# Optimization experiments

Measured on AMD Instinct MI355X. Metric: run time of the kernel, lower is better.

The kernel has to match this reference:

```python
import jax, jax.numpy as jnp
from jax import lax
import numpy as np

B, S, V, E, H, K = 128, 512, 32000, 128, 128, 32  # H = hidden_dim//2 per direction
START, END = 30, 31


def _lstm_dir(x, h0, c0, W_ih, W_hh, b):
    # x: [S, B, E]; PyTorch gate order: i, f, g, o
    def step(carry, xt):
        h, c = carry
        gates = xt @ W_ih.T + h @ W_hh.T + b  # [B, 4H]
        i, f, g, o = jnp.split(gates, 4, axis=1)
        c = jax.nn.sigmoid(f) * c + jax.nn.sigmoid(i) * jnp.tanh(g)
        h = jax.nn.sigmoid(o) * jnp.tanh(c)
        return (h, c), h
    _, hs = lax.scan(step, (h0, c0), x)
    return hs  # [S, B, H]


def _get_features(sentence, embed_table, W_ih_f, W_hh_f, b_ih_f, b_hh_f,
                  W_ih_b, W_hh_b, b_ih_b, b_hh_b, W_out, b_out, h0, c0):
    emb = embed_table[sentence]            # [B, S, E]
    x = emb.transpose(1, 0, 2)             # [S, B, E]
    hf = _lstm_dir(x, h0[0], c0[0], W_ih_f, W_hh_f, b_ih_f + b_hh_f)
    hb = _lstm_dir(x[::-1], h0[1], c0[1], W_ih_b, W_hh_b, b_ih_b + b_hh_b)[::-1]
    out = jnp.concatenate([hf, hb], axis=-1).transpose(1, 0, 2)  # [B, S, 2H]
    return out @ W_out.T + b_out           # [B, S, K]


def _numerator(feats, tags, transitions):
    b = tags.shape[0]
    start = jnp.full((b, 1), START, dtype=tags.dtype)
    ext = jnp.concatenate([start, tags], axis=1)  # [B, S+1]
    trans = transitions[ext[:, :-1], ext[:, 1:]].sum(axis=1)
    emit = jnp.take_along_axis(feats, tags[:, :, None], axis=2)[..., 0].sum(axis=1)
    return trans + emit + transitions[tags[:, -1], END]


def _denominator(feats, transitions):
    b, _, k = feats.shape
    init = jnp.full((b, k), -10000.0, feats.dtype).at[:, START].set(0.0)
    def step(alpha, feat):
        # alpha[b, prev]; transitions[next, prev] (as in the torch code)
        new = jax.nn.logsumexp(alpha[:, None, :] + transitions[None, :, :], axis=2) + feat
        return new, None
    alpha, _ = lax.scan(step, init, feats.transpose(1, 0, 2))
    return jax.nn.logsumexp(alpha + transitions[:, END][None, :], axis=1)


def setup_inputs():
    key = jax.random.key(0)
    ks = jax.random.split(key, 16)
    n = lambda k, shape, s=0.1: jax.random.normal(k, shape, jnp.float32) * s
    sentence = jax.random.randint(ks[0], (B, S), 0, V)
    tags = jax.random.randint(ks[1], (B, S), 0, START)
    transitions = n(ks[13], (K, K), 0.1)
    transitions = transitions.at[:, START].set(-10000.0).at[END, :].set(-10000.0)
    return dict(
        sentence=sentence, tags=tags,
        embed_table=n(ks[2], (V, E), 1.0),
        W_ih_f=n(ks[3], (4 * H, E)), W_hh_f=n(ks[4], (4 * H, H)),
        b_ih_f=n(ks[5], (4 * H,)), b_hh_f=n(ks[6], (4 * H,)),
        W_ih_b=n(ks[7], (4 * H, E)), W_hh_b=n(ks[8], (4 * H, H)),
        b_ih_b=n(ks[9], (4 * H,)), b_hh_b=n(ks[10], (4 * H,)),
        W_out=n(ks[11], (K, 2 * H)), b_out=n(ks[12], (K,)),
        transitions=transitions,
        h0=n(ks[14], (2, B, H)), c0=n(ks[15], (2, B, H)),
    )


def reference(sentence, tags, embed_table, W_ih_f, W_hh_f, b_ih_f, b_hh_f,
              W_ih_b, W_hh_b, b_ih_b, b_hh_b, W_out, b_out, transitions, h0, c0):
    feats = _get_features(sentence, embed_table, W_ih_f, W_hh_f, b_ih_f, b_hh_f,
                          W_ih_b, W_hh_b, b_ih_b, b_hh_b, W_out, b_out, h0, c0)
    num = _numerator(feats, tags, transitions)
    den = _denominator(feats, transitions)
    return jnp.mean(num - den)
```

## Files before the change

### kernel.cpp

```cpp
#include <hip/hip_runtime.h>

typedef unsigned int uint;
typedef unsigned short ushort;
typedef __fp16 half2_t __attribute__((ext_vector_type(2)));
typedef __fp16 half8_t __attribute__((ext_vector_type(8)));
typedef float floatx4 __attribute__((ext_vector_type(4)));

#define SEQ 512
#define BATCH 128
#define HID 128
#define NTAG 32
#define START_TAG 30
#define END_TAG 31

__device__ __forceinline__ float fdot2(uint a, uint b, float c) {
  return __builtin_amdgcn_fdot2(__builtin_bit_cast(half2_t, a),
                                __builtin_bit_cast(half2_t, b), c, false);
}
__device__ __forceinline__ uint packh2(float a, float b) {
  half2_t h = __builtin_amdgcn_cvt_pkrtz(a, b);
  return __builtin_bit_cast(uint, h);
}
__device__ __forceinline__ float frcp(float x) { return __builtin_amdgcn_rcpf(x); }
__device__ __forceinline__ float fexp2(float x) { return __builtin_amdgcn_exp2f(x); }
__device__ __forceinline__ float flog2(float x) { return __builtin_amdgcn_logf(x); }

__device__ __forceinline__ float quad_add(float x) {
  int a = __builtin_bit_cast(int, x);
  int b = __builtin_amdgcn_update_dpp(0, a, 0xB1, 0xF, 0xF, true);
  float y = x + __builtin_bit_cast(float, b);
  int c2 = __builtin_bit_cast(int, y);
  int d2 = __builtin_amdgcn_update_dpp(0, c2, 0x4E, 0xF, 0xF, true);
  return y + __builtin_bit_cast(float, d2);
}
template <int CTRL>
__device__ __forceinline__ float quad_bcast(float x) {
  int a = __builtin_bit_cast(int, x);
  int b = __builtin_amdgcn_update_dpp(0, a, CTRL, 0xF, 0xF, true);
  return __builtin_bit_cast(float, b);
}

__global__ __launch_bounds__(256) void prep_kernel(
    const float* __restrict__ Wihf, const float* __restrict__ Whhf,
    const float* __restrict__ bihf, const float* __restrict__ bhhf,
    const float* __restrict__ Wihb, const float* __restrict__ Whhb,
    const float* __restrict__ bihb, const float* __restrict__ bhhb,
    const float* __restrict__ Wout, const int* __restrict__ sentence,
    const float* __restrict__ embed,
    uint* __restrict__ wihI, uint* __restrict__ whh,
    uint* __restrict__ woutp, float* __restrict__ biasI,
    int* __restrict__ sentT, uint* __restrict__ embH)
{
  int idx = blockIdx.x * 256 + threadIdx.x;
  if (idx < 65536) {
    int d = idx >> 15, rem = idx & 32767;
    int n = rem >> 6, dw = rem & 63;
    int m = n >> 2, q = n & 3;
    int g = q * 128 + m;
    const float* W = d ? Wihb : Wihf;
    wihI[idx] = packh2(W[g * 128 + 2 * dw], W[g * 128 + 2 * dw + 1]);
  }
  int i2 = idx - 65536;
  if (i2 >= 0 && i2 < 65536) {
    int d = i2 >> 15, rem = i2 & 32767;
    int g = rem >> 6, dw = rem & 63;
    const float* W = d ? Whhb : Whhf;
    whh[i2] = packh2(W[g * 128 + 2 * dw], W[g * 128 + 2 * dw + 1]);
  }
  int i3 = idx - 131072;
  if (i3 >= 0 && i3 < 4096) {
    int k = i3 >> 7, dw = i3 & 127;
    float a, b2;
    if (dw < 64) { a = Wout[k * 256 + 2 * dw]; b2 = Wout[k * 256 + 2 * dw + 1]; }
    else { int j = dw - 64; a = Wout[k * 256 + 128 + 2 * j]; b2 = Wout[k * 256 + 128 + 2 * j + 1]; }
    woutp[i3] = packh2(a, b2);
  }
  int i4 = idx - 135168;
  if (i4 >= 0 && i4 < 1024) {
    int d = i4 >> 9, n = i4 & 511;
    int g = (n & 3) * 128 + (n >> 2);
    biasI[i4] = d ? (bihb[g] + bhhb[g]) : (bihf[g] + bhhf[g]);
  }
  int i5 = idx - 136192;
  if (i5 >= 0 && i5 < 65536) {
    int b = i5 & 127, s = i5 >> 7;
    sentT[i5] = sentence[b * SEQ + s];
  }
  int i6 = idx - 201728;
  if (i6 >= 0 && i6 < 2097152) {
    embH[i6] = packh2(embed[2 * i6], embed[2 * i6 + 1]);
  }
}

template <bool ALLT>
__device__ __forceinline__ void gemmx_body(
    const int* __restrict__ sentT, const float* __restrict__ embed,
    const uint* __restrict__ embH,
    const uint* __restrict__ wihI, const float* __restrict__ biasI,
    uint* __restrict__ gatex, int chunk, int blk)
{
  int tl = blk & 127, nb = (blk >> 7) & 3, d = blk >> 9;
  int t = chunk * 128 + tl;
  int s = d ? (511 - t) : t;
  __shared__ int tok[128];
  __shared__ __align__(16) __fp16 tile[128][136];
  int tid = threadIdx.x;
  if (tid < 128) tok[tid] = sentT[s * 128 + tid];
  __syncthreads();

  int w = tid >> 6, lane = tid & 63;
  int q = lane >> 4, r = lane & 15;
  int wr = w >> 1, wc = w & 1;
  int r0 = wr * 64;
  int cl0 = wc * 64;
  int c0 = nb * 128 + cl0;

  floatx4 acc[4][4];
#pragma unroll
  for (int i = 0; i < 4; ++i)
#pragma unroll
    for (int j = 0; j < 4; ++j) acc[i][j] = (floatx4){0.f, 0.f, 0.f, 0.f};

  const uint4* bptr[4];
#pragma unroll
  for (int j = 0; j < 4; ++j)
    bptr[j] = (const uint4*)(wihI + ((size_t)d * 512 + c0 + j * 16 + r) * 64) + q;

  if constexpr (ALLT) {
    const uint4* aptr[4];
#pragma unroll
    for (int i = 0; i < 4; ++i)
      aptr[i] = (const uint4*)embH + (size_t)tok[r0 + i * 16 + r] * 16 + q;
#pragma unroll
    for (int kc = 0; kc < 4; ++kc) {
      half8_t af[4], bf[4];
#pragma unroll
      for (int i = 0; i < 4; ++i)
        af[i] = __builtin_bit_cast(half8_t, aptr[i][kc * 4]);
#pragma unroll
      for (int j = 0; j < 4; ++j)
        bf[j] = __builtin_bit_cast(half8_t, bptr[j][kc * 4]);
#pragma unroll
      for (int i = 0; i < 4; ++i)
#pragma unroll
        for (int j = 0; j < 4; ++j)
          acc[i][j] = __builtin_amdgcn_mfma_f32_16x16x32_f16(af[i], bf[j], acc[i][j], 0, 0, 0);
    }
  } else {
    const float4* aptr[4];
#pragma unroll
    for (int i = 0; i < 4; ++i)
      aptr[i] = (const float4*)(embed + (size_t)tok[r0 + i * 16 + r] * HID) + q * 2;
#pragma unroll
    for (int kc = 0; kc < 4; ++kc) {
      half8_t af[4], bf[4];
#pragma unroll
      for (int i = 0; i < 4; ++i) {
        float4 x0 = aptr[i][kc * 8];
        float4 x1 = aptr[i][kc * 8 + 1];
        uint4 u;
        u.x = packh2(x0.x, x0.y); u.y = packh2(x0.z, x0.w);
        u.z = packh2(x1.x, x1.y); u.w = packh2(x1.z, x1.w);
        af[i] = __builtin_bit_cast(half8_t, u);
      }
#pragma unroll
      for (int j = 0; j < 4; ++j)
        bf[j] = __builtin_bit_cast(half8_t, bptr[j][kc * 4]);
#pragma unroll
      for (int i = 0; i < 4; ++i)
#pragma unroll
        for (int j = 0; j < 4; ++j)
          acc[i][j] = __builtin_amdgcn_mfma_f32_16x16x32_f16(af[i], bf[j], acc[i][j], 0, 0, 0);
    }
  }

#pragma unroll
  for (int j = 0; j < 4; ++j) {
    int cl = cl0 + j * 16 + r;
    float bb = biasI[d * 512 + nb * 128 + cl];
#pragma unroll
    for (int i = 0; i < 4; ++i) {
      int rb = r0 + i * 16 + q * 4;
#pragma unroll
      for (int reg = 0; reg < 4; ++reg)
        tile[rb + reg][cl] = (__fp16)(acc[i][j][reg] + bb);
    }
  }
  __syncthreads();

  size_t dstride = ALLT ? (size_t)65536 * 512 : (size_t)16384 * 512;
  int rowbase = (ALLT ? t : tl) * 128;
  __fp16* gat = ((__fp16*)gatex) + (size_t)d * dstride;
  int prow = tid >> 4, pseg = tid & 15;
#pragma unroll
  for (int pass = 0; pass < 8; ++pass) {
    int row = pass * 16 + prow;
    uint4 v = *(const uint4*)(&tile[row][pseg * 8]);
    *(uint4*)(gat + ((size_t)(rowbase + row)) * 512 + nb * 128 + pseg * 8) = v;
  }
}

__global__ __launch_bounds__(256, 2) void gemmx_kernel(
    const int* __restrict__ sentT, const float* __restrict__ embed,
    const uint* __restrict__ wihI, const float* __restrict__ biasI,
    uint* __restrict__ gatex, int chunk)
{
  gemmx_body<false>(sentT, embed, nullptr, wihI, biasI, gatex, chunk, blockIdx.x);
}

__global__ __launch_bounds__(256, 2) void gemmx_all_kernel(
    const int* __restrict__ sentT, const uint* __restrict__ embH,
    const uint* __restrict__ wihI, const float* __restrict__ biasI,
    uint* __restrict__ gatex)
{
  gemmx_body<true>(sentT, nullptr, embH, wihI, biasI, gatex,
                   blockIdx.x >> 10, blockIdx.x & 1023);
}

struct LstmCtx {
  uint4 wreg[4][4];
  float sl, Ac, Bc;
  int kq, m;
};

__device__ __forceinline__ void lstm_step(
    LstmCtx& cx, __fp16 (*hist)[128], int row_r, int row_w, ushort gxh,
    float& c)
{
  const float L2E = 1.4426950408889634f;
  float a0 = 0.f, a1 = 0.f, a2 = 0.f, a3 = 0.f;
  float b0 = 0.f, b1 = 0.f, b2 = 0.f, b3 = 0.f;
  const uint4* z4 = (const uint4*)(&hist[row_r][cx.kq * 32]);
#pragma unroll
  for (int i = 0; i < 2; ++i) {
    uint4 z = z4[i];
    a0 = fdot2(z.x, cx.wreg[0][i].x, a0);
    a0 = fdot2(z.y, cx.wreg[0][i].y, a0);
    a0 = fdot2(z.z, cx.wreg[0][i].z, a0);
    a0 = fdot2(z.w, cx.wreg[0][i].w, a0);
    a1 = fdot2(z.x, cx.wreg[1][i].x, a1);
    a1 = fdot2(z.y, cx.wreg[1][i].y, a1);
    a1 = fdot2(z.z, cx.wreg[1][i].z, a1);
    a1 = fdot2(z.w, cx.wreg[1][i].w, a1);
    a2 = fdot2(z.x, cx.wreg[2][i].x, a2);
    a2 = fdot2(z.y, cx.wreg[2][i].y, a2);
    a2 = fdot2(z.z, cx.wreg[2][i].z, a2);
    a2 = fdot2(z.w, cx.wreg[2][i].w, a2);
    a3 = fdot2(z.x, cx.wreg[3][i].x, a3);
    a3 = fdot2(z.y, cx.wreg[3][i].y, a3);
    a3 = fdot2(z.z, cx.wreg[3][i].z, a3);
    a3 = fdot2(z.w, cx.wreg[3][i].w, a3);
  }
#pragma unroll
  for (int i = 2; i < 4; ++i) {
    uint4 z = z4[i];
    b0 = fdot2(z.x, cx.wreg[0][i].x, b0);
    b0 = fdot2(z.y, cx.wreg[0][i].y, b0);
    b0 = fdot2(z.z, cx.wreg[0][i].z, b0);
    b0 = fdot2(z.w, cx.wreg[0][i].w, b0);
    b1 = fdot2(z.x, cx.wreg[1][i].x, b1);
    b1 = fdot2(z.y, cx.wreg[1][i].y, b1);
    b1 = fdot2(z.z, cx.wreg[1][i].z, b1);
    b1 = fdot2(z.w, cx.wreg[1][i].w, b1);
    b2 = fdot2(z.x, cx.wreg[2][i].x, b2);
    b2 = fdot2(z.y, cx.wreg[2][i].y, b2);
    b2 = fdot2(z.z, cx.wreg[2][i].z, b2);
    b2 = fdot2(z.w, cx.wreg[2][i].w, b2);
    b3 = fdot2(z.x, cx.wreg[3][i].x, b3);
    b3 = fdot2(z.y, cx.wreg[3][i].y, b3);
    b3 = fdot2(z.z, cx.wreg[3][i].z, b3);
    b3 = fdot2(z.w, cx.wreg[3][i].w, b3);
  }
  a0 += b0; a1 += b1; a2 += b2; a3 += b3;
  a0 = quad_add(a0);
  a1 = quad_add(a1);
  a2 = quad_add(a2);
  a3 = quad_add(a3);
  float s01 = (cx.kq & 1) ? a1 : a0;
  float s23 = (cx.kq & 1) ? a3 : a2;
  float own = (cx.kq & 2) ? s23 : s01;
  own += (float)__builtin_bit_cast(__fp16, gxh);
  float e = fexp2(own * cx.sl);
  float r = frcp(1.f + e);
  float out = cx.Ac * r + cx.Bc;
  float ig = quad_bcast<0x00>(out);
  float fg = quad_bcast<0x55>(out);
  float gg = quad_bcast<0xAA>(out);
  float og = quad_bcast<0xFF>(out);
  c = fg * c + ig * gg;
  float e2 = fexp2(c * (2.f * L2E));
  float r2 = frcp(1.f + e2);
  float th = 1.f - 2.f * r2;
  float hv = og * th;

  if (cx.kq == 0) hist[row_w][cx.m] = (__fp16)hv;
  __builtin_amdgcn_sched_barrier(0);
  asm volatile("s_waitcnt lgkmcnt(0)");
  __builtin_amdgcn_sched_barrier(0);
  __builtin_amdgcn_s_barrier();
}

__device__ __forceinline__ void lstm_init(LstmCtx& cx, const uint* whh,
                                          int d, int tid)
{
  const float L2E = 1.4426950408889634f;
  cx.kq = tid & 3;
  cx.m = tid >> 2;
  const bool isg = (cx.kq == 2);
  cx.sl = isg ? (2.f * L2E) : (-L2E);
  cx.Ac = isg ? -2.f : 1.f;
  cx.Bc = isg ? 1.f : 0.f;
  const uint4* wh4 = (const uint4*)whh + (size_t)d * 8192;
#pragma unroll
  for (int g = 0; g < 4; ++g) {
    const uint4* row = wh4 + ((size_t)(g * 128 + cx.m)) * 16 + cx.kq * 4;
#pragma unroll
    for (int i = 0; i < 4; ++i) cx.wreg[g][i] = row[i];
  }
}

__global__ __attribute__((amdgpu_waves_per_eu(2, 2))) __launch_bounds__(512)
void lstm_kernel(
    const uint* __restrict__ gatex, const uint* __restrict__ whh,
    const float* __restrict__ h0, const float* __restrict__ c0,
    float* __restrict__ statec, uint* __restrict__ hh, int chunk)
{
  const int wg = blockIdx.x;
  const int d = wg >> 7, b = wg & 127;
  const int tid = threadIdx.x;

  __shared__ __align__(16) __fp16 hist[128][128];
  LstmCtx cx;
  lstm_init(cx, whh, d, tid);

  float c = (chunk == 0) ? c0[(size_t)(d * 128 + b) * 128 + cx.m]
                         : statec[(size_t)(d * 128 + b) * 128 + cx.m];

  if (tid < 64) {
    uint* h127 = (uint*)&hist[127][0];
    if (chunk == 0) {
      float2 hv = ((const float2*)(h0 + (size_t)(d * 128 + b) * 128))[tid];
      h127[tid] = packh2(hv.x, hv.y);
    } else {
      int sprev = d ? (511 - (chunk * 128 - 1)) : (chunk * 128 - 1);
      h127[tid] = hh[((size_t)(d * 512 + sprev) * 128 + b) * 64 + tid];
    }
  }
  const ushort* gxp = (const ushort*)gatex + (size_t)d * 8388608 +
                      (size_t)b * 512 + 4 * cx.m + cx.kq;

  ushort g0 = gxp[0];
  ushort g1 = gxp[(size_t)1 * 65536];
  ushort g2 = gxp[(size_t)2 * 65536];
  ushort g3 = gxp[(size_t)3 * 65536];
  __syncthreads();

  for (int tl = 0; tl < 128; tl += 4) {
    int i0 = tl + 4 > 127 ? 127 : tl + 4;
    int i1 = tl + 5 > 127 ? 127 : tl + 5;
    int i2 = tl + 6 > 127 ? 127 : tl + 6;
    int i3 = tl + 7 > 127 ? 127 : tl + 7;
    ushort n0 = gxp[(size_t)i0 * 65536];
    ushort n1 = gxp[(size_t)i1 * 65536];
    ushort n2 = gxp[(size_t)i2 * 65536];
    ushort n3 = gxp[(size_t)i3 * 65536];
    lstm_step(cx, hist, (tl + 127) & 127, tl + 0, g0, c);
    lstm_step(cx, hist, (tl + 0) & 127, tl + 1, g1, c);
    lstm_step(cx, hist, (tl + 1) & 127, tl + 2, g2, c);
    lstm_step(cx, hist, (tl + 2) & 127, tl + 3, g3, c);
    g0 = n0; g1 = n1; g2 = n2; g3 = n3;
  }

  if (cx.kq == 0) statec[(size_t)(d * 128 + b) * 128 + cx.m] = c;

  int base = chunk * 128;
  for (int i = tid; i < 2048; i += 512) {
    int sl2 = i >> 4, q4 = i & 15;
    int s = d ? (511 - (base + sl2)) : (base + sl2);
    *(uint4*)(&hh[((size_t)(d * 512 + s) * 128 + b) * 64 + q4 * 4]) =
        *(const uint4*)((const uint*)&hist[sl2][0] + q4 * 4);
  }
}

__global__ __attribute__((amdgpu_waves_per_eu(2, 2))) __launch_bounds__(512)
void lstm_all_kernel(
    const uint* __restrict__ gatex, const uint* __restrict__ whh,
    const float* __restrict__ h0, const float* __restrict__ c0,
    uint* __restrict__ hh)
{
  const int wg = blockIdx.x;
  const int d = wg >> 7, b = wg & 127;
  const int tid = threadIdx.x;

  __shared__ __align__(16) __fp16 hist[128][128];
  LstmCtx cx;
  lstm_init(cx, whh, d, tid);

  float c = c0[(size_t)(d * 128 + b) * 128 + cx.m];

  if (tid < 64) {
    uint* h127 = (uint*)&hist[127][0];
    float2 hv = ((const float2*)(h0 + (size_t)(d * 128 + b) * 128))[tid];
    h127[tid] = packh2(hv.x, hv.y);
  }
  const ushort* gxp = (const ushort*)gatex + (size_t)d * 33554432 +
                      (size_t)b * 512 + 4 * cx.m + cx.kq;

  ushort g0 = gxp[0];
  ushort g1 = gxp[(size_t)1 * 65536];
  ushort g2 = gxp[(size_t)2 * 65536];
  ushort g3 = gxp[(size_t)3 * 65536];
  __syncthreads();

  for (int tl = 0; tl < 512; tl += 4) {
    int i0 = tl + 4 > 511 ? 511 : tl + 4;
    int i1 = tl + 5 > 511 ? 511 : tl + 5;
    int i2 = tl + 6 > 511 ? 511 : tl + 6;
    int i3 = tl + 7 > 511 ? 511 : tl + 7;
    ushort n0 = gxp[(size_t)i0 * 65536];
    ushort n1 = gxp[(size_t)i1 * 65536];
    ushort n2 = gxp[(size_t)i2 * 65536];
    ushort n3 = gxp[(size_t)i3 * 65536];
    lstm_step(cx, hist, (tl + 127) & 127, (tl + 0) & 127, g0, c);
    lstm_step(cx, hist, (tl + 0) & 127, (tl + 1) & 127, g1, c);
    lstm_step(cx, hist, (tl + 1) & 127, (tl + 2) & 127, g2, c);
    lstm_step(cx, hist, (tl + 2) & 127, (tl + 3) & 127, g3, c);
    g0 = n0; g1 = n1; g2 = n2; g3 = n3;

    if (((tl + 3) & 127) == 127) {
      int base = ((tl + 3) >> 7) * 128;
      for (int i = tid; i < 2048; i += 512) {
        int sl2 = i >> 4, q4 = i & 15;
        int s = d ? (511 - (base + sl2)) : (base + sl2);
        *(uint4*)(&hh[((size_t)(d * 512 + s) * 128 + b) * 64 + q4 * 4]) =
            *(const uint4*)((const uint*)&hist[sl2][0] + q4 * 4);
      }
      __syncthreads();
    }
  }
}

__global__ __launch_bounds__(256) void outproj_kernel(
    const uint* __restrict__ hh, const uint* __restrict__ woutp,
    const float* __restrict__ bout, float* __restrict__ feats)
{
  int tid = threadIdx.x;
  int w = tid >> 6, lane = tid & 63;
  int q = lane >> 4, c = lane & 15;
  int row0 = blockIdx.x * 64 + w * 16;

  const uint4* wp4 = (const uint4*)woutp;
  uint4 bf0[8], bf1[8];
#pragma unroll
  for (int ks = 0; ks < 8; ++ks) {
    bf0[ks] = wp4[(size_t)c * 32 + ks * 4 + q];
    bf1[ks] = wp4[(size_t)(16 + c) * 32 + ks * 4 + q];
  }

  int rr = row0 + c;
  int br = rr >> 9, sr = rr & 511;
  const uint4* af4 = (const uint4*)(hh + ((size_t)(sr * BATCH + br)) * 64);
  const uint4* ab4 = (const uint4*)(hh + ((size_t)((SEQ + sr) * BATCH + br)) * 64);

  floatx4 acc0 = (floatx4){0.f, 0.f, 0.f, 0.f};
  floatx4 acc1 = (floatx4){0.f, 0.f, 0.f, 0.f};
#pragma unroll
  for (int ks = 0; ks < 8; ++ks) {
    uint4 a = (ks < 4) ? af4[ks * 4 + q] : ab4[(ks - 4) * 4 + q];
    half8_t af = __builtin_bit_cast(half8_t, a);
    acc0 = __builtin_amdgcn_mfma_f32_16x16x32_f16(
        af, __builtin_bit_cast(half8_t, bf0[ks]), acc0, 0, 0, 0);
    acc1 = __builtin_amdgcn_mfma_f32_16x16x32_f16(
        af, __builtin_bit_cast(half8_t, bf1[ks]), acc1, 0, 0, 0);
  }

  float bb0 = bout[c], bb1 = bout[16 + c];
#pragma unroll
  for (int reg = 0; reg < 4; ++reg) {
    int orow = row0 + q * 4 + reg;
    feats[(size_t)orow * 32 + c] = acc0[reg] + bb0;
    feats[(size_t)orow * 32 + 16 + c] = acc1[reg] + bb1;
  }
}

__global__ __launch_bounds__(64) void crf_seg_kernel(
    const float* __restrict__ feats, const float* __restrict__ trans,
    uint* __restrict__ segP, float* __restrict__ segL)
{
  const float L2E = 1.4426950408889634f;
  int blk = blockIdx.x;
  int b = blk >> 5, j = blk & 31;
  int tstart = 1 + 16 * j;
  int nsteps = (j == 31) ? 15 : 16;
  int lane = threadIdx.x;
  int c = lane & 15, q = lane >> 4;

  half8_t afr[2];
#pragma unroll
  for (int rt = 0; rt < 2; ++rt) {
    const float* trow = trans + (rt * 16 + c) * 32 + q * 8;
    float e[8];
#pragma unroll
    for (int i = 0; i < 8; ++i) e[i] = fexp2(trow[i] * L2E);
    uint4 u;
    u.x = packh2(e[0], e[1]); u.y = packh2(e[2], e[3]);
    u.z = packh2(e[4], e[5]); u.w = packh2(e[6], e[7]);
    afr[rt] = __builtin_bit_cast(half8_t, u);
  }
  half8_t bfr[2];
#pragma unroll
  for (int ct = 0; ct < 2; ++ct) {
    uint4 u;
    uint vals[8];
#pragma unroll
    for (int i = 0; i < 8; ++i)
      vals[i] = ((q * 8 + i) == (ct * 16 + c)) ? 0x3C00u : 0u;
    u.x = vals[0] | (vals[1] << 16);
    u.y = vals[2] | (vals[3] << 16);
    u.z = vals[4] | (vals[5] << 16);
    u.w = vals[6] | (vals[7] << 16);
    bfr[ct] = __builtin_bit_cast(half8_t, u);
  }

  __shared__ __fp16 P16[32 * 36];

  const float* fb = feats + ((size_t)b * SEQ + tstart) * NTAG;
  float Lacc = 0.f;
  float4 pre0 = *(const float4*)(fb + q * 4);
  float4 pre1 = *(const float4*)(fb + 16 + q * 4);

  for (int s = 0; s < nsteps; ++s) {
    float4 f0 = pre0, f1 = pre1;
    if (s + 1 < nsteps) {
      pre0 = *(const float4*)(fb + (s + 1) * 32 + q * 4);
      pre1 = *(const float4*)(fb + (s + 1) * 32 + 16 + q * 4);
    }
    floatx4 z4 = (floatx4){0.f, 0.f, 0.f, 0.f};
    floatx4 c00 = __builtin_amdgcn_mfma_f32_16x16x32_f16(afr[0], bfr[0], z4, 0, 0, 0);
    floatx4 c01 = __builtin_amdgcn_mfma_f32_16x16x32_f16(afr[0], bfr[1], z4, 0, 0, 0);
    floatx4 c10 = __builtin_amdgcn_mfma_f32_16x16x32_f16(afr[1], bfr[0], z4, 0, 0, 0);
    floatx4 c11 = __builtin_amdgcn_mfma_f32_16x16x32_f16(afr[1], bfr[1], z4, 0, 0, 0);
    float pf0[4], pf1[4];
    pf0[0] = fexp2(f0.x * L2E); pf0[1] = fexp2(f0.y * L2E);
    pf0[2] = fexp2(f0.z * L2E); pf0[3] = fexp2(f0.w * L2E);
    pf1[0] = fexp2(f1.x * L2E); pf1[1] = fexp2(f1.y * L2E);
    pf1[2] = fexp2(f1.z * L2E); pf1[3] = fexp2(f1.w * L2E);
    float v00[4], v01[4], v10[4], v11[4];
#pragma unroll
    for (int rg = 0; rg < 4; ++rg) {
      v00[rg] = c00[rg] * pf0[rg];
      v01[rg] = c01[rg] * pf0[rg];
      v10[rg] = c10[rg] * pf1[rg];
      v11[rg] = c11[rg] * pf1[rg];
    }
    float mx = 0.f;
#pragma unroll
    for (int rg = 0; rg < 4; ++rg)
      mx = fmaxf(mx, fmaxf(fmaxf(v00[rg], v01[rg]), fmaxf(v10[rg], v11[rg])));
    uint ub = (uint)__builtin_amdgcn_readfirstlane((int)__builtin_bit_cast(uint, mx));
    int e = (int)((ub >> 23) & 255u);
    Lacc += (float)(e - 127);
    float sc = __builtin_bit_cast(float, (uint)((254 - e) << 23));

    __syncthreads();
    {
      uint2 wv2;
      wv2.x = packh2(v00[0] * sc, v00[1] * sc);
      wv2.y = packh2(v00[2] * sc, v00[3] * sc);
      *(uint2*)(&P16[c * 36 + q * 4]) = wv2;
      wv2.x = packh2(v10[0] * sc, v10[1] * sc);
      wv2.y = packh2(v10[2] * sc, v10[3] * sc);
      *(uint2*)(&P16[c * 36 + 16 + q * 4]) = wv2;
      wv2.x = packh2(v01[0] * sc, v01[1] * sc);
      wv2.y = packh2(v01[2] * sc, v01[3] * sc);
      *(uint2*)(&P16[(16 + c) * 36 + q * 4]) = wv2;
      wv2.x = packh2(v11[0] * sc, v11[1] * sc);
      wv2.y = packh2(v11[2] * sc, v11[3] * sc);
      *(uint2*)(&P16[(16 + c) * 36 + 16 + q * 4]) = wv2;
    }
    __syncthreads();
    {
      uint2 lo0 = *(const uint2*)(&P16[c * 36 + q * 8]);
      uint2 hi0 = *(const uint2*)(&P16[c * 36 + q * 8 + 4]);
      uint4 u0; u0.x = lo0.x; u0.y = lo0.y; u0.z = hi0.x; u0.w = hi0.y;
      bfr[0] = __builtin_bit_cast(half8_t, u0);
      uint2 lo1 = *(const uint2*)(&P16[(16 + c) * 36 + q * 8]);
      uint2 hi1 = *(const uint2*)(&P16[(16 + c) * 36 + q * 8 + 4]);
      uint4 u1; u1.x = lo1.x; u1.y = lo1.y; u1.z = hi1.x; u1.w = hi1.y;
      bfr[1] = __builtin_bit_cast(half8_t, u1);
    }
  }
  __syncthreads();
  uint* gp = segP + (size_t)blk * 512;
  if (lane < 32) {
    int i = lane;
#pragma unroll
    for (int tp = 0; tp < 16; ++tp) {
      uint lo = (uint)__builtin_bit_cast(unsigned short, P16[(2 * tp) * 36 + i]);
      uint hi = (uint)__builtin_bit_cast(unsigned short, P16[(2 * tp + 1) * 36 + i]);
      gp[i * 16 + tp] = lo | (hi << 16);
    }
  }
  if (lane == 0) segL[blk] = Lacc;
}

__global__ __launch_bounds__(64) void crf_comb_kernel(
    const int* __restrict__ tags, const float* __restrict__ feats,
    const float* __restrict__ trans, const uint* __restrict__ segP,
    const float* __restrict__ segL, float* __restrict__ num,
    float* __restrict__ den)
{
  const float L2E = 1.4426950408889634f, LN2 = 0.6931471805599453f;
  int b = blockIdx.x, l = threadIdx.x;

  {
    const int* tb = tags + b * SEQ;
    float acc = 0.f;
    for (int s = l; s < SEQ; s += 64) {
      int tg = tb[s];
      int pv = (s == 0) ? START_TAG : tb[s - 1];
      acc += trans[pv * NTAG + tg] + feats[((size_t)b * SEQ + s) * NTAG + tg];
    }
#pragma unroll
    for (int msk = 1; msk < 64; msk <<= 1) acc += __shfl_xor(acc, msk);
    if (l == 0) num[b] = acc + trans[tb[SEQ - 1] * NTAG + END_TAG];
  }

  int i = l & 31, hp = l >> 5;
  const float* fb = feats + (size_t)b * SEQ * NTAG;

  float sT = 0.f;
  for (int p = 0; p < 32; ++p) sT += fexp2(trans[i * 32 + p] * L2E);
  float v = (1.f + sT) * fexp2(fb[i] * L2E);
  float L = -10000.f * L2E;

  float vo = __shfl_xor(v, 1);
  uint pv = (i & 1) ? packh2(vo, v) : packh2(v, vo);

  const uint* gp0 = segP + (size_t)b * 32 * 512 + i * 16 + hp * 8;
  uint4 ra = *(const uint4*)(gp0);
  uint4 rb = *(const uint4*)(gp0 + 4);

  for (int seg = 0; seg < 32; ++seg) {
    uint4 ca = ra, cb = rb;
    if (seg + 1 < 32) {
      ra = *(const uint4*)(gp0 + (seg + 1) * 512);
      rb = *(const uint4*)(gp0 + (seg + 1) * 512 + 4);
    }
    float g0 = __shfl(__builtin_bit_cast(float, pv), hp * 16 + 0);
    float g1 = __shfl(__builtin_bit_cast(float, pv), hp * 16 + 2);
    float g2 = __shfl(__builtin_bit_cast(float, pv), hp * 16 + 4);
    float g3 = __shfl(__builtin_bit_cast(float, pv), hp * 16 + 6);
    float g4 = __shfl(__builtin_bit_cast(float, pv), hp * 16 + 8);
    float g5 = __shfl(__builtin_bit_cast(float, pv), hp * 16 + 10);
    float g6 = __shfl(__builtin_bit_cast(float, pv), hp * 16 + 12);
    float g7 = __shfl(__builtin_bit_cast(float, pv), hp * 16 + 14);
    float acc = 0.f;
    acc = fdot2(__builtin_bit_cast(uint, g0), ca.x, acc);
    acc = fdot2(__builtin_bit_cast(uint, g1), ca.y, acc);
    acc = fdot2(__builtin_bit_cast(uint, g2), ca.z, acc);
    acc = fdot2(__builtin_bit_cast(uint, g3), ca.w, acc);
    acc = fdot2(__builtin_bit_cast(uint, g4), cb.x, acc);
    acc = fdot2(__builtin_bit_cast(uint, g5), cb.y, acc);
    acc = fdot2(__builtin_bit_cast(uint, g6), cb.z, acc);
    acc = fdot2(__builtin_bit_cast(uint, g7), cb.w, acc);
    float sm = acc + __shfl_xor(acc, 32);
    uint ub = (uint)__builtin_amdgcn_readfirstlane((int)__builtin_bit_cast(uint, sm));
    int e = (int)((ub >> 23) & 255u);
    L += (float)(e - 127) + segL[b * 32 + seg];
    float sc = __builtin_bit_cast(float, (uint)((254 - e) << 23));
    v = sm * sc;
    float vo2 = __shfl_xor(v, 1);
    pv = (i & 1) ? packh2(vo2, v) : packh2(v, vo2);
  }
  float wv = v * fexp2(trans[i * 32 + END_TAG] * L2E);
#pragma unroll
  for (int msk = 1; msk <= 16; msk <<= 1) wv += __shfl_xor(wv, msk);
  if (l == 0) den[b] = (L + flog2(wv)) * LN2;
}

__global__ __launch_bounds__(128) void final_kernel(
    const float* __restrict__ num, const float* __restrict__ den,
    float* __restrict__ out)
{
  int tid = threadIdx.x;
  float v = num[tid] - den[tid];
#pragma unroll
  for (int msk = 1; msk < 64; msk <<= 1) v += __shfl_xor(v, msk);
  __shared__ float tmp[2];
  if ((tid & 63) == 0) tmp[tid >> 6] = v;
  __syncthreads();
  if (tid == 0) out[0] = (tmp[0] + tmp[1]) * (1.f / 128.f);
}

extern "C" void kernel_launch(void* const* d_in, const int* in_sizes, int n_in,
                              void* d_out, int out_size, void* d_ws, size_t ws_size,
                              hipStream_t stream)
{
  const int* sentence = (const int*)d_in[0];
  const int* tags = (const int*)d_in[1];
  const float* embed = (const float*)d_in[2];
  const float* Wihf = (const float*)d_in[3];
  const float* Whhf = (const float*)d_in[4];
  const float* bihf = (const float*)d_in[5];
  const float* bhhf = (const float*)d_in[6];
  const float* Wihb = (const float*)d_in[7];
  const float* Whhb = (const float*)d_in[8];
  const float* bihb = (const float*)d_in[9];
  const float* bhhb = (const float*)d_in[10];
  const float* Wout = (const float*)d_in[11];
  const float* bout = (const float*)d_in[12];
  const float* trans = (const float*)d_in[13];
  const float* h0 = (const float*)d_in[14];
  const float* c0 = (const float*)d_in[15];
  float* out = (float*)d_out;

  char* ws = (char*)d_ws;
  uint* wihI = (uint*)(ws + 0);
  uint* whh = (uint*)(ws + 262144);
  uint* woutp = (uint*)(ws + 524288);
  float* biasI = (float*)(ws + 540672);
  float* numb = (float*)(ws + 544768);
  float* denb = (float*)(ws + 545280);
  float* statec = (float*)(ws + 545792);
  int* sentT = (int*)(ws + 700416);
  uint* hh = (uint*)(ws + 1048576);
  uint* embH = (uint*)(ws + 1048576);
  uint* gatex = (uint*)(ws + 34603008);
  float* feats = (float*)(ws + 34603008);
  uint* segP = (uint*)(ws + 42991616);
  float* segL = (float*)(ws + 51380224);

  hipLaunchKernelGGL(prep_kernel, dim3(8980), dim3(256), 0, stream,
                     Wihf, Whhf, bihf, bhhf, Wihb, Whhb, bihb, bhhb, Wout,
                     sentence, embed, wihI, whh, woutp, biasI, sentT, embH);

  bool big = ws_size >= 168820736ull;
  if (big) {
    hipLaunchKernelGGL(gemmx_all_kernel, dim3(4096), dim3(256), 0, stream,
                       sentT, embH, wihI, biasI, gatex);
    hipLaunchKernelGGL(lstm_all_kernel, dim3(256), dim3(512), 0, stream,
                       gatex, whh, h0, c0, hh);
  } else {
    for (int c = 0; c < 4; ++c) {
      hipLaunchKernelGGL(gemmx_kernel, dim3(1024), dim3(256), 0, stream,
                         sentT, embed, wihI, biasI, gatex, c);
      hipLaunchKernelGGL(lstm_kernel, dim3(256), dim3(512), 0, stream,
                         gatex, whh, h0, c0, statec, hh, c);
    }
  }

  hipLaunchKernelGGL(outproj_kernel, dim3(1024), dim3(256), 0, stream,
                     hh, woutp, bout, feats);
  hipLaunchKernelGGL(crf_seg_kernel, dim3(4096), dim3(64), 0, stream,
                     feats, trans, segP, segL);
  hipLaunchKernelGGL(crf_comb_kernel, dim3(128), dim3(64), 0, stream,
                     tags, feats, trans, segP, segL, numb, denb);
  hipLaunchKernelGGL(final_kernel, dim3(1), dim3(128), 0, stream,
                     numb, denb, out);
}
```

Before: 483.1 us.

## Process two batch rows per LSTM workgroup with interleaved recurrent steps

Each LSTM workgroup now runs two independent batch sequences at once, using a paired step that interleaves their dot products, gate activations and hidden-state writes. It keeps a separate shared-memory history buffer per sequence and launches half as many workgroups. The aim is to hide the latency of each serial recurrent step with instruction-level parallelism and to share each per-step barrier and the register-resident weights across two sequences. In exchange each step does twice the work and the grid drops to 128 workgroups, which may leave compute units idle and lengthen the per-step critical path.

```diff
diff --git a/kernel.cpp b/kernel.cpp
--- a/kernel.cpp
+++ b/kernel.cpp
@@ -222,6 +222,25 @@
   float sl, Ac, Bc;
   int kq, m;
 };
+
+__device__ __forceinline__ void lstm_init(LstmCtx& cx, const uint* whh,
+                                          int d, int tid)
+{
+  const float L2E = 1.4426950408889634f;
+  cx.kq = tid & 3;
+  cx.m = tid >> 2;
+  const bool isg = (cx.kq == 2);
+  cx.sl = isg ? (2.f * L2E) : (-L2E);
+  cx.Ac = isg ? -2.f : 1.f;
+  cx.Bc = isg ? 1.f : 0.f;
+  const uint4* wh4 = (const uint4*)whh + (size_t)d * 8192;
+#pragma unroll
+  for (int g = 0; g < 4; ++g) {
+    const uint4* row = wh4 + ((size_t)(g * 128 + cx.m)) * 16 + cx.kq * 4;
+#pragma unroll
+    for (int i = 0; i < 4; ++i) cx.wreg[g][i] = row[i];
+  }
+}
 
 __device__ __forceinline__ void lstm_step(
     LstmCtx& cx, __fp16 (*hist)[128], int row_r, int row_w, ushort gxh,
@@ -300,23 +319,99 @@
   __builtin_amdgcn_s_barrier();
 }
 
-__device__ __forceinline__ void lstm_init(LstmCtx& cx, const uint* whh,
-                                          int d, int tid)
+__device__ __forceinline__ void lstm_step2(
+    LstmCtx& cx, __fp16 (*histA)[128], __fp16 (*histB)[128],
+    int row_r, int row_w, ushort gxa, ushort gxb, float& ca, float& cb)
 {
   const float L2E = 1.4426950408889634f;
-  cx.kq = tid & 3;
-  cx.m = tid >> 2;
-  const bool isg = (cx.kq == 2);
-  cx.sl = isg ? (2.f * L2E) : (-L2E);
-  cx.Ac = isg ? -2.f : 1.f;
-  cx.Bc = isg ? 1.f : 0.f;
-  const uint4* wh4 = (const uint4*)whh + (size_t)d * 8192;
-#pragma unroll
-  for (int g = 0; g < 4; ++g) {
-    const uint4* row = wh4 + ((size_t)(g * 128 + cx.m)) * 16 + cx.kq * 4;
-#pragma unroll
-    for (int i = 0; i < 4; ++i) cx.wreg[g][i] = row[i];
-  }
+  float a0 = 0.f, a1 = 0.f, a2 = 0.f, a3 = 0.f;
+  float e0 = 0.f, e1 = 0.f, e2 = 0.f, e3 = 0.f;
+  const uint4* zA4 = (const uint4*)(&histA[row_r][cx.kq * 32]);
+  const uint4* zB4 = (const uint4*)(&histB[row_r][cx.kq * 32]);
+#pragma unroll
+  for (int i = 0; i < 4; ++i) {
+    uint4 zA = zA4[i];
+    uint4 zB = zB4[i];
+    a0 = fdot2(zA.x, cx.wreg[0][i].x, a0);
+    e0 = fdot2(zB.x, cx.wreg[0][i].x, e0);
+    a0 = fdot2(zA.y, cx.wreg[0][i].y, a0);
+    e0 = fdot2(zB.y, cx.wreg[0][i].y, e0);
+    a0 = fdot2(zA.z, cx.wreg[0][i].z, a0);
+    e0 = fdot2(zB.z, cx.wreg[0][i].z, e0);
+    a0 = fdot2(zA.w, cx.wreg[0][i].w, a0);
+    e0 = fdot2(zB.w, cx.wreg[0][i].w, e0);
+    a1 = fdot2(zA.x, cx.wreg[1][i].x, a1);
+    e1 = fdot2(zB.x, cx.wreg[1][i].x, e1);
+    a1 = fdot2(zA.y, cx.wreg[1][i].y, a1);
+    e1 = fdot2(zB.y, cx.wreg[1][i].y, e1);
+    a1 = fdot2(zA.z, cx.wreg[1][i].z, a1);
+    e1 = fdot2(zB.z, cx.wreg[1][i].z, e1);
+    a1 = fdot2(zA.w, cx.wreg[1][i].w, a1);
+    e1 = fdot2(zB.w, cx.wreg[1][i].w, e1);
+    a2 = fdot2(zA.x, cx.wreg[2][i].x, a2);
+    e2 = fdot2(zB.x, cx.wreg[2][i].x, e2);
+    a2 = fdot2(zA.y, cx.wreg[2][i].y, a2);
+    e2 = fdot2(zB.y, cx.wreg[2][i].y, e2);
+    a2 = fdot2(zA.z, cx.wreg[2][i].z, a2);
+    e2 = fdot2(zB.z, cx.wreg[2][i].z, e2);
+    a2 = fdot2(zA.w, cx.wreg[2][i].w, a2);
+    e2 = fdot2(zB.w, cx.wreg[2][i].w, e2);
+    a3 = fdot2(zA.x, cx.wreg[3][i].x, a3);
+    e3 = fdot2(zB.x, cx.wreg[3][i].x, e3);
+    a3 = fdot2(zA.y, cx.wreg[3][i].y, a3);
+    e3 = fdot2(zB.y, cx.wreg[3][i].y, e3);
+    a3 = fdot2(zA.z, cx.wreg[3][i].z, a3);
+    e3 = fdot2(zB.z, cx.wreg[3][i].z, e3);
+    a3 = fdot2(zA.w, cx.wreg[3][i].w, a3);
+    e3 = fdot2(zB.w, cx.wreg[3][i].w, e3);
+  }
+  a0 = quad_add(a0);
+  e0 = quad_add(e0);
+  a1 = quad_add(a1);
+  e1 = quad_add(e1);
+  a2 = quad_add(a2);
+  e2 = quad_add(e2);
+  a3 = quad_add(a3);
+  e3 = quad_add(e3);
+  float sA01 = (cx.kq & 1) ? a1 : a0;
+  float sB01 = (cx.kq & 1) ? e1 : e0;
+  float sA23 = (cx.kq & 1) ? a3 : a2;
+  float sB23 = (cx.kq & 1) ? e3 : e2;
+  float ownA = (cx.kq & 2) ? sA23 : sA01;
+  float ownB = (cx.kq & 2) ? sB23 : sB01;
+  ownA += (float)__builtin_bit_cast(__fp16, gxa);
+  ownB += (float)__builtin_bit_cast(__fp16, gxb);
+  float eA = fexp2(ownA * cx.sl);
+  float eB = fexp2(ownB * cx.sl);
+  float rA = frcp(1.f + eA);
+  float rB = frcp(1.f + eB);
+  float outA = cx.Ac * rA + cx.Bc;
+  float outB = cx.Ac * rB + cx.Bc;
+  float igA = quad_bcast<0x00>(outA);
+  float igB = quad_bcast<0x00>(outB);
+  float fgA = quad_bcast<0x55>(outA);
+  float fgB = quad_bcast<0x55>(outB);
+  float ggA = quad_bcast<0xAA>(outA);
+  float ggB = quad_bcast<0xAA>(outB);
+  float ogA = quad_bcast<0xFF>(outA);
+  float ogB = quad_bcast<0xFF>(outB);
+  ca = fgA * ca + igA * ggA;
+  cb = fgB * cb + igB * ggB;
+  float e2A = fexp2(ca * (2.f * L2E));
+  float e2B = fexp2(cb * (2.f * L2E));
+  float r2A = frcp(1.f + e2A);
+  float r2B = frcp(1.f + e2B);
+  float hvA = ogA * (1.f - 2.f * r2A);
+  float hvB = ogB * (1.f - 2.f * r2B);
+
+  if (cx.kq == 0) {
+    histA[row_w][cx.m] = (__fp16)hvA;
+    histB[row_w][cx.m] = (__fp16)hvB;
+  }
+  __builtin_amdgcn_sched_barrier(0);
+  asm volatile("s_waitcnt lgkmcnt(0)");
+  __builtin_amdgcn_sched_barrier(0);
+  __builtin_amdgcn_s_barrier();
 }
 
 __global__ __attribute__((amdgpu_waves_per_eu(2, 2))) __launch_bounds__(512)
@@ -389,27 +484,31 @@
     uint* __restrict__ hh)
 {
   const int wg = blockIdx.x;
-  const int d = wg >> 7, b = wg & 127;
+  const int d = wg >> 6, bpair = wg & 63;
+  const int b0 = bpair * 2;
   const int tid = threadIdx.x;
 
-  __shared__ __align__(16) __fp16 hist[128][128];
+  __shared__ __align__(16) __fp16 hist[2][128][128];
   LstmCtx cx;
   lstm_init(cx, whh, d, tid);
 
-  float c = c0[(size_t)(d * 128 + b) * 128 + cx.m];
-
-  if (tid < 64) {
-    uint* h127 = (uint*)&hist[127][0];
-    float2 hv = ((const float2*)(h0 + (size_t)(d * 128 + b) * 128))[tid];
-    h127[tid] = packh2(hv.x, hv.y);
-  }
-  const ushort* gxp = (const ushort*)gatex + (size_t)d * 33554432 +
-                      (size_t)b * 512 + 4 * cx.m + cx.kq;
-
-  ushort g0 = gxp[0];
-  ushort g1 = gxp[(size_t)1 * 65536];
-  ushort g2 = gxp[(size_t)2 * 65536];
-  ushort g3 = gxp[(size_t)3 * 65536];
+  float ca = c0[(size_t)(d * 128 + b0) * 128 + cx.m];
+  float cb = c0[(size_t)(d * 128 + b0 + 1) * 128 + cx.m];
+
+  if (tid < 128) {
+    int p = tid >> 6, t6 = tid & 63;
+    uint* h127 = (uint*)&hist[p][127][0];
+    float2 hv = ((const float2*)(h0 + (size_t)(d * 128 + b0 + p) * 128))[t6];
+    h127[t6] = packh2(hv.x, hv.y);
+  }
+  const ushort* gxp0 = (const ushort*)gatex + (size_t)d * 33554432 +
+                       (size_t)b0 * 512 + 4 * cx.m + cx.kq;
+  const ushort* gxp1 = gxp0 + 512;
+
+  ushort ga0 = gxp0[0], gb0 = gxp1[0];
+  ushort ga1 = gxp0[(size_t)1 * 65536], gb1 = gxp1[(size_t)1 * 65536];
+  ushort ga2 = gxp0[(size_t)2 * 65536], gb2 = gxp1[(size_t)2 * 65536];
+  ushort ga3 = gxp0[(size_t)3 * 65536], gb3 = gxp1[(size_t)3 * 65536];
   __syncthreads();
 
   for (int tl = 0; tl < 512; tl += 4) {
@@ -417,23 +516,25 @@
     int i1 = tl + 5 > 511 ? 511 : tl + 5;
     int i2 = tl + 6 > 511 ? 511 : tl + 6;
     int i3 = tl + 7 > 511 ? 511 : tl + 7;
-    ushort n0 = gxp[(size_t)i0 * 65536];
-    ushort n1 = gxp[(size_t)i1 * 65536];
-    ushort n2 = gxp[(size_t)i2 * 65536];
-    ushort n3 = gxp[(size_t)i3 * 65536];
-    lstm_step(cx, hist, (tl + 127) & 127, (tl + 0) & 127, g0, c);
-    lstm_step(cx, hist, (tl + 0) & 127, (tl + 1) & 127, g1, c);
-    lstm_step(cx, hist, (tl + 1) & 127, (tl + 2) & 127, g2, c);
-    lstm_step(cx, hist, (tl + 2) & 127, (tl + 3) & 127, g3, c);
-    g0 = n0; g1 = n1; g2 = n2; g3 = n3;
+    ushort na0 = gxp0[(size_t)i0 * 65536], nb0 = gxp1[(size_t)i0 * 65536];
+    ushort na1 = gxp0[(size_t)i1 * 65536], nb1 = gxp1[(size_t)i1 * 65536];
+    ushort na2 = gxp0[(size_t)i2 * 65536], nb2 = gxp1[(size_t)i2 * 65536];
+    ushort na3 = gxp0[(size_t)i3 * 65536], nb3 = gxp1[(size_t)i3 * 65536];
+    lstm_step2(cx, hist[0], hist[1], (tl + 127) & 127, (tl + 0) & 127, ga0, gb0, ca, cb);
+    lstm_step2(cx, hist[0], hist[1], (tl + 0) & 127, (tl + 1) & 127, ga1, gb1, ca, cb);
+    lstm_step2(cx, hist[0], hist[1], (tl + 1) & 127, (tl + 2) & 127, ga2, gb2, ca, cb);
+    lstm_step2(cx, hist[0], hist[1], (tl + 2) & 127, (tl + 3) & 127, ga3, gb3, ca, cb);
+    ga0 = na0; ga1 = na1; ga2 = na2; ga3 = na3;
+    gb0 = nb0; gb1 = nb1; gb2 = nb2; gb3 = nb3;
 
     if (((tl + 3) & 127) == 127) {
       int base = ((tl + 3) >> 7) * 128;
-      for (int i = tid; i < 2048; i += 512) {
-        int sl2 = i >> 4, q4 = i & 15;
+      for (int i = tid; i < 4096; i += 512) {
+        int p2 = i >> 11, r2i = i & 2047;
+        int sl2 = r2i >> 4, q4 = r2i & 15;
         int s = d ? (511 - (base + sl2)) : (base + sl2);
-        *(uint4*)(&hh[((size_t)(d * 512 + s) * 128 + b) * 64 + q4 * 4]) =
-            *(const uint4*)((const uint*)&hist[sl2][0] + q4 * 4);
+        *(uint4*)(&hh[((size_t)(d * 512 + s) * 128 + (b0 + p2)) * 64 + q4 * 4]) =
+            *(const uint4*)((const uint*)&hist[p2][sl2][0] + q4 * 4);
       }
       __syncthreads();
     }
@@ -739,7 +840,7 @@
   if (big) {
     hipLaunchKernelGGL(gemmx_all_kernel, dim3(4096), dim3(256), 0, stream,
                        sentT, embH, wihI, biasI, gatex);
-    hipLaunchKernelGGL(lstm_all_kernel, dim3(256), dim3(512), 0, stream,
+    hipLaunchKernelGGL(lstm_all_kernel, dim3(128), dim3(512), 0, stream,
                        gatex, whh, h0, c0, hh);
   } else {
     for (int c = 0; c < 4; ++c) {
```

Result: slower. 665.2 us (+37.7%).
